# Performance work log

Hardware: AMD Instinct MI355X
Metric: run time of the kernel (lower is better)

The kernel has to match this reference:

```python
import jax, jax.numpy as jnp
from jax import lax
import numpy as np

EPS = 1e-5   # BatchNorm eps (torch default)
LAM = 0.01
W_SIZE = 32768  # window_size; fc_features = W_SIZE - 1


def _conv(x, w, b):
    # torch Conv1d, valid padding; x [N,C,L], w [O,I,K]
    y = lax.conv_general_dilated(x, w, (1,), 'VALID', dimension_numbers=('NCH', 'OIH', 'NCH'))
    return y + b[None, :, None]


def _convT(x, w, b):
    # torch ConvTranspose1d stride 1, pad 0 == full conv with flipped, axis-swapped kernel
    # w [I,O,K] (torch layout) -> [O,I,K] flipped
    k = w.shape[-1]
    wt = jnp.flip(jnp.swapaxes(w, 0, 1), -1)
    y = lax.conv_general_dilated(x, wt, (1,), [(k - 1, k - 1)], dimension_numbers=('NCH', 'OIH', 'NCH'))
    return y + b[None, :, None]


def _bn(x, g, b):
    # BatchNorm1d in training mode: batch stats over (N, L), biased variance
    mu = x.mean((0, 2), keepdims=True)
    var = x.var((0, 2), keepdims=True)
    return g[None, :, None] * (x - mu) * lax.rsqrt(var + EPS) + b[None, :, None]


def setup_inputs() -> dict:
    key = jax.random.key(0)
    ks = jax.random.split(key, 12)
    W = W_SIZE
    F = W - 1
    def w(k, shape):
        return jax.random.normal(k, shape, jnp.float32) * 0.02
    return {
        'x': jax.random.normal(ks[0], (1, 1, 33), jnp.float32),
        'e1_w': w(ks[1], (256, 1, 3)), 'e1_b': jnp.zeros(256),
        'bn2_g': jnp.ones(256), 'bn2_b': jnp.zeros(256),
        'e2_w': w(ks[2], (128, 256, 3)), 'e2_b': jnp.zeros(128),
        'bn3_g': jnp.ones(128), 'bn3_b': jnp.zeros(128),
        'e3_w': w(ks[3], (64, 128, 3)), 'e3_b': jnp.zeros(64),
        'bn4_g': jnp.ones(64), 'bn4_b': jnp.zeros(64),
        'e4_w': w(ks[4], (32, 64, 3)), 'e4_b': jnp.zeros(32),
        'efc_w': w(ks[5], (W, 800)), 'efc_b': jnp.zeros(W),
        'dfc_w': w(ks[6], (800, F)), 'dfc_b': jnp.zeros(800),
        'dbn4_g': jnp.ones(32), 'dbn4_b': jnp.zeros(32),
        'd4_w': w(ks[7], (32, 64, 5)), 'd4_b': jnp.zeros(64),
        'dbn3_g': jnp.ones(64), 'dbn3_b': jnp.zeros(64),
        'd3_w': w(ks[8], (64, 128, 5)), 'd3_b': jnp.zeros(128),
        'dbn2_g': jnp.ones(128), 'dbn2_b': jnp.zeros(128),
        'd2_w': w(ks[9], (128, 256, 5)), 'd2_b': jnp.zeros(256),
        'dbn1_g': jnp.ones(256), 'dbn1_b': jnp.zeros(256),
        'd1_w': w(ks[10], (256, 1, 3)), 'd1_b': jnp.zeros(1),
    }


def reference(x, e1_w, e1_b, bn2_g, bn2_b, e2_w, e2_b, bn3_g, bn3_b, e3_w, e3_b,
              bn4_g, bn4_b, e4_w, e4_b, efc_w, efc_b, dfc_w, dfc_b,
              dbn4_g, dbn4_b, d4_w, d4_b, dbn3_g, dbn3_b, d3_w, d3_b,
              dbn2_g, dbn2_b, d2_w, d2_b, dbn1_g, dbn1_b, d1_w, d1_b):
    # ---- encoder ----
    h = _conv(x, e1_w, e1_b)                                   # [1,256,31]
    h = _conv(jax.nn.relu(_bn(h, bn2_g, bn2_b)), e2_w, e2_b)   # [1,128,29]
    h = _conv(jax.nn.relu(_bn(h, bn3_g, bn3_b)), e3_w, e3_b)   # [1,64,27]
    h = _conv(_bn(jax.nn.relu(h), bn4_g, bn4_b), e4_w, e4_b)   # [1,32,25]
    z = h.reshape(1, -1) @ efc_w.T + efc_b                     # [1, W]
    # ---- calc_Ytilde_prd (no control) ----
    v = z.reshape(-1)
    X, Y = v[:-1], v[1:]                                       # [W-1]
    # m>=n branch: Af = pinv(X^T X + lam) @ X^T Y ; X^T X + lam > 0 so pinv = reciprocal
    Af = jnp.dot(X, Y) / (jnp.dot(X, X) + jnp.asarray(LAM, v.dtype))
    n = X.shape[0]
    # linear scalar recurrence y_i = X[0] * Af^i, vectorized via cumprod
    powers = jnp.cumprod(jnp.concatenate([jnp.ones((1,), v.dtype), jnp.full((n - 1,), Af)]))
    out2 = jnp.stack([X, X[0] * powers], axis=0)               # [2, W-1]
    # ---- decoder ----
    d = out2 @ dfc_w.T + dfc_b                                 # [2, 800]
    d = d.reshape(32, -1)[None]                                # [1,32,50]
    d = _convT(jax.nn.relu(_bn(d, dbn4_g, dbn4_b)), d4_w, d4_b)  # [1,64,54]
    d = _convT(_bn(jax.nn.relu(d), dbn3_g, dbn3_b), d3_w, d3_b)  # [1,128,58]
    d = _convT(_bn(jax.nn.relu(d), dbn2_g, dbn2_b), d2_w, d2_b)  # [1,256,62]
    d = _convT(jax.nn.relu(_bn(d, dbn1_g, dbn1_b)), d1_w, d1_b)  # [1,1,64]
    return jnp.squeeze(d)                                      # [64]
```

## Files before the change

kernel.cpp:

```cpp
#include <hip/hip_runtime.h>
#include <math.h>

#define EPS 1e-5f

__device__ __forceinline__ float waveReduceSum(float v) {
#pragma unroll
    for (int off = 32; off > 0; off >>= 1) v += __shfl_xor(v, off, 64);
    return v;
}

template <int IC, int OC, int LIN, int LOUT, bool BN_FIRST, bool STATS_RELU>
__global__ __launch_bounds__(256) void enc_conv(const float* __restrict__ xin,
                                                const float* __restrict__ g, const float* __restrict__ bb,
                                                const float* __restrict__ s, const float* __restrict__ q,
                                                const float* __restrict__ w, const float* __restrict__ bias,
                                                float* __restrict__ out,
                                                float* __restrict__ so, float* __restrict__ qo) {
    __shared__ float sc[IC], sh[IC];
    int t = threadIdx.x;
    for (int ic = t; ic < IC; ic += 256) {
        float mean = s[ic] / (float)LIN;
        float var = q[ic] / (float)LIN - mean * mean;
        float scale = g[ic] * rsqrtf(var + EPS);
        sc[ic] = scale; sh[ic] = bb[ic] - mean * scale;
    }
    __syncthreads();
    int o = blockIdx.x * 4 + (t >> 6);
    int lane = t & 63;
    if (o >= OC * LOUT) return;
    int oc = o / LOUT, p = o % LOUT;
    constexpr int TERMS = IC * 3;
    const float* wr = w + oc * TERMS;
    float acc = 0.f;
#pragma unroll
    for (int i = 0; i < (TERMS + 63) / 64; i++) {
        int j = 64 * i + lane;
        if ((TERMS & 63) && j >= TERMS) break;
        int ic = j / 3, k = j - ic * 3;
        float xv = xin[ic * LIN + p + k];
        float v;
        if (BN_FIRST) { v = xv * sc[ic] + sh[ic]; v = v > 0.f ? v : 0.f; }
        else          { xv = xv > 0.f ? xv : 0.f; v = xv * sc[ic] + sh[ic]; }
        acc += v * wr[j];
    }
    acc = waveReduceSum(acc);
    if (lane == 0) {
        acc += bias[oc];
        out[oc * LOUT + p] = acc;
        if (so) {
            float r = STATS_RELU ? (acc > 0.f ? acc : 0.f) : acc;
            atomicAdd(&so[oc], r); atomicAdd(&qo[oc], r * r);
        }
    }
}

template <int IC, int OC, int LIN, int LOUT, bool BN_FIRST, bool STATS_RELU>
__global__ __launch_bounds__(256) void dec_convt(const float* __restrict__ xin,
                                                 const float* __restrict__ g, const float* __restrict__ bb,
                                                 const float* __restrict__ s, const float* __restrict__ q,
                                                 const float* __restrict__ w, const float* __restrict__ bias,
                                                 float* __restrict__ out,
                                                 float* __restrict__ so, float* __restrict__ qo) {
    __shared__ float sc[IC], sh[IC];
    int t = threadIdx.x;
    for (int ic = t; ic < IC; ic += 256) {
        float mean = s[ic] / (float)LIN;
        float var = q[ic] / (float)LIN - mean * mean;
        float scale = g[ic] * rsqrtf(var + EPS);
        sc[ic] = scale; sh[ic] = bb[ic] - mean * scale;
    }
    __syncthreads();
    int o = blockIdx.x * 4 + (t >> 6);
    int lane = t & 63;
    if (o >= OC * LOUT) return;
    int oc = o / LOUT, p = o % LOUT;
    constexpr int TERMS = IC * 5;
    float acc = 0.f;
#pragma unroll
    for (int i = 0; i < (TERMS + 63) / 64; i++) {
        int j = 64 * i + lane;
        if ((TERMS & 63) && j >= TERMS) break;
        int ic = j / 5, kk = j - ic * 5;
        int m = p - kk;
        if (m >= 0 && m < LIN) {
            float xv = xin[ic * LIN + m];
            float v;
            if (BN_FIRST) { v = xv * sc[ic] + sh[ic]; v = v > 0.f ? v : 0.f; }
            else          { xv = xv > 0.f ? xv : 0.f; v = xv * sc[ic] + sh[ic]; }
            acc += v * w[ic * (OC * 5) + oc * 5 + kk];
        }
    }
    acc = waveReduceSum(acc);
    if (lane == 0) {
        acc += bias[oc];
        out[oc * LOUT + p] = acc;
        if (so) {
            float r = STATS_RELU ? (acc > 0.f ? acc : 0.f) : acc;
            atomicAdd(&so[oc], r); atomicAdd(&qo[oc], r * r);
        }
    }
}

__global__ __launch_bounds__(256) void k2_enc12(const float* __restrict__ x,
                                                const float* __restrict__ w1,
                                                const float* __restrict__ b1,
                                                const float* __restrict__ g2,
                                                const float* __restrict__ bb2,
                                                const float* __restrict__ w2,
                                                const float* __restrict__ b2,
                                                float* __restrict__ h2,
                                                float* __restrict__ s3, float* __restrict__ q3) {
    __shared__ float xs[33];
    __shared__ float w1l[768];
    __shared__ float b1l[256];
    __shared__ float sc2[256], sh2[256];
    int t = threadIdx.x;
    if (t < 33) xs[t] = x[t];
    for (int i = t; i < 768; i += 256) w1l[i] = w1[i];
    b1l[t] = b1[t];
    __syncthreads();
    {
        float w0 = w1l[t * 3], wa = w1l[t * 3 + 1], wb = w1l[t * 3 + 2], bias = b1l[t];
        float s = 0.f, q = 0.f;
#pragma unroll
        for (int pp = 0; pp < 31; pp++) {
            float v = xs[pp] * w0 + xs[pp + 1] * wa + xs[pp + 2] * wb + bias;
            s += v; q += v * v;
        }
        float mean = s / 31.f;
        float var = q / 31.f - mean * mean;
        float scale = g2[t] * rsqrtf(var + EPS);
        sc2[t] = scale; sh2[t] = bb2[t] - mean * scale;
    }
    __syncthreads();
    int o = blockIdx.x * 4 + (t >> 6);
    int lane = t & 63;
    int oc = o / 29, p = o % 29;
    const float* wr = w2 + oc * 768;
    float acc = 0.f;
#pragma unroll
    for (int i = 0; i < 12; i++) {
        int j = 64 * i + lane;
        int ic = j / 3, k = j - ic * 3;
        int pos = p + k;
        float e1v = xs[pos] * w1l[ic * 3] + xs[pos + 1] * w1l[ic * 3 + 1] + xs[pos + 2] * w1l[ic * 3 + 2] + b1l[ic];
        float v = e1v * sc2[ic] + sh2[ic];
        v = v > 0.f ? v : 0.f;
        acc += v * wr[j];
    }
    acc = waveReduceSum(acc);
    if (lane == 0) {
        acc += b2[oc];
        h2[oc * 29 + p] = acc;
        atomicAdd(&s3[oc], acc);
        atomicAdd(&q3[oc], acc * acc);
    }
}

__global__ __launch_bounds__(256) void k5_gemv1(const float* __restrict__ w,
                                                const float* __restrict__ h,
                                                const float* __restrict__ b,
                                                float* __restrict__ z) {
    int wave = threadIdx.x >> 6;
    int lane = threadIdx.x & 63;
    int row = blockIdx.x * 4 + wave;
    const float4* wr = (const float4*)(w + (size_t)row * 800);
    const float4* hv = (const float4*)h;
    float acc = 0.f;
#pragma unroll
    for (int t = 0; t < 3; t++) {
        float4 a = wr[lane + 64 * t];
        float4 c = hv[lane + 64 * t];
        acc += a.x * c.x + a.y * c.y + a.z * c.z + a.w * c.w;
    }
    if (lane < 8) {
        float4 a = wr[192 + lane];
        float4 c = hv[192 + lane];
        acc += a.x * c.x + a.y * c.y + a.z * c.z + a.w * c.w;
    }
    acc = waveReduceSum(acc);
    if (lane == 0) z[row] = acc + b[row];
}

__global__ __launch_bounds__(1024) void k67_afpow(const float* __restrict__ z, float* __restrict__ pw) {
    int t = threadIdx.x;
    const float4* z4 = (const float4*)z;
    float xy = 0.f, xx = 0.f;
    for (int v = t; v < 8191; v += 1024) {
        float4 a = z4[v];
        float nb = z[4 * v + 4];
        xy += a.x * a.y + a.y * a.z + a.z * a.w + a.w * nb;
        xx += a.x * a.x + a.y * a.y + a.z * a.z + a.w * a.w;
    }
    if (t < 3) {
        int i = 32764 + t;
        xy += z[i] * z[i + 1];
        xx += z[i] * z[i];
    }
    xy = waveReduceSum(xy);
    xx = waveReduceSum(xx);
    __shared__ float sx[16], sy[16];
    __shared__ float afs;
    int wv = t >> 6, ln = t & 63;
    if (ln == 0) { sy[wv] = xy; sx[wv] = xx; }
    __syncthreads();
    if (t == 0) {
        float SY = 0.f, SX = 0.f;
        for (int i = 0; i < 16; i++) { SY += sy[i]; SX += sx[i]; }
        afs = SY / (SX + 0.01f);
    }
    __syncthreads();
    float base0 = afs;
    float4* pw4 = (float4*)pw;
    for (int v = t; v < 8192; v += 1024) {
        float4 r;
        float* rp = (float*)&r;
#pragma unroll
        for (int u = 0; u < 4; u++) {
            int e = 4 * v + u;
            float rr = 1.f, base = base0;
            while (e) { if (e & 1) rr *= base; base *= base; e >>= 1; }
            rp[u] = rr;
        }
        pw4[v] = r;
    }
}

__global__ __launch_bounds__(256) void k8_gemv2(const float* __restrict__ w,
                                                const float* __restrict__ z,
                                                const float* __restrict__ pw,
                                                const float* __restrict__ b,
                                                float* __restrict__ d,
                                                float* __restrict__ s, float* __restrict__ q) {
    int j = blockIdx.x;
    int t = threadIdx.x;
    const float* wr = w + (size_t)j * 32767;
    int head = j & 3;
    float a0 = 0.f, a1 = 0.f;
    if (t < head) { float wv = wr[t]; a0 += z[t] * wv; a1 += pw[t] * wv; }
    int n4 = (32767 - head) >> 2;
    const float4* wv4 = (const float4*)(wr + head);
    for (int v = t; v < n4; v += 256) {
        float4 a = wv4[v];
        int i = head + 4 * v;
        a0 += z[i] * a.x + z[i + 1] * a.y + z[i + 2] * a.z + z[i + 3] * a.w;
        a1 += pw[i] * a.x + pw[i + 1] * a.y + pw[i + 2] * a.z + pw[i + 3] * a.w;
    }
    int tail = (32767 - head) & 3;
    int tstart = head + 4 * n4;
    if (t < tail) { int i = tstart + t; float wv = wr[i]; a0 += z[i] * wv; a1 += pw[i] * wv; }

    a0 = waveReduceSum(a0);
    a1 = waveReduceSum(a1);
    __shared__ float r0[4], r1[4];
    int wave = t >> 6, lane = t & 63;
    if (lane == 0) { r0[wave] = a0; r1[wave] = a1; }
    __syncthreads();
    if (t == 0) {
        float d0 = r0[0] + r0[1] + r0[2] + r0[3] + b[j];
        float d1 = z[0] * (r1[0] + r1[1] + r1[2] + r1[3]) + b[j];
        d[j] = d0;
        d[800 + j] = d1;
        int c0 = j / 50, c1 = 16 + j / 50;
        atomicAdd(&s[c0], d0); atomicAdd(&q[c0], d0 * d0);
        atomicAdd(&s[c1], d1); atomicAdd(&q[c1], d1 * d1);
    }
}

__global__ __launch_bounds__(256) void k12_dec1(const float* __restrict__ h6,
                                                const float* __restrict__ g, const float* __restrict__ bb,
                                                const float* __restrict__ s, const float* __restrict__ q,
                                                const float* __restrict__ w, const float* __restrict__ b1,
                                                float* __restrict__ out) {
    __shared__ float sc[256], sh[256];
    int t = threadIdx.x;
    {
        float mean = s[t] / 62.f;
        float var = q[t] / 62.f - mean * mean;
        float scale = g[t] * rsqrtf(var + EPS);
        sc[t] = scale; sh[t] = bb[t] - mean * scale;
    }
    __syncthreads();
    int p = blockIdx.x * 4 + (t >> 6);
    int lane = t & 63;
    float acc = 0.f;
#pragma unroll
    for (int i = 0; i < 12; i++) {
        int j = 64 * i + lane;
        int ic = j / 3, kk = j - ic * 3;
        int m = p - kk;
        if (m >= 0 && m < 62) {
            float v = h6[ic * 62 + m] * sc[ic] + sh[ic];
            v = v > 0.f ? v : 0.f;
            acc += v * w[j];
        }
    }
    acc = waveReduceSum(acc);
    if (lane == 0) out[p] = acc + b1[0];
}

extern "C" void kernel_launch(void* const* d_in, const int* in_sizes, int n_in,
                              void* d_out, int out_size, void* d_ws, size_t ws_size,
                              hipStream_t stream) {
    const float* x      = (const float*)d_in[0];
    const float* e1_w   = (const float*)d_in[1];
    const float* e1_b   = (const float*)d_in[2];
    const float* bn2_g  = (const float*)d_in[3];
    const float* bn2_b  = (const float*)d_in[4];
    const float* e2_w   = (const float*)d_in[5];
    const float* e2_b   = (const float*)d_in[6];
    const float* bn3_g  = (const float*)d_in[7];
    const float* bn3_b  = (const float*)d_in[8];
    const float* e3_w   = (const float*)d_in[9];
    const float* e3_b   = (const float*)d_in[10];
    const float* bn4_g  = (const float*)d_in[11];
    const float* bn4_b  = (const float*)d_in[12];
    const float* e4_w   = (const float*)d_in[13];
    const float* e4_b   = (const float*)d_in[14];
    const float* efc_w  = (const float*)d_in[15];
    const float* efc_b  = (const float*)d_in[16];
    const float* dfc_w  = (const float*)d_in[17];
    const float* dfc_b  = (const float*)d_in[18];
    const float* dbn4_g = (const float*)d_in[19];
    const float* dbn4_b = (const float*)d_in[20];
    const float* d4_w   = (const float*)d_in[21];
    const float* d4_b   = (const float*)d_in[22];
    const float* dbn3_g = (const float*)d_in[23];
    const float* dbn3_b = (const float*)d_in[24];
    const float* d3_w   = (const float*)d_in[25];
    const float* d3_b   = (const float*)d_in[26];
    const float* dbn2_g = (const float*)d_in[27];
    const float* dbn2_b = (const float*)d_in[28];
    const float* d2_w   = (const float*)d_in[29];
    const float* d2_b   = (const float*)d_in[30];
    const float* dbn1_g = (const float*)d_in[31];
    const float* dbn1_b = (const float*)d_in[32];
    const float* d1_w   = (const float*)d_in[33];
    const float* d1_b   = (const float*)d_in[34];
    float* out = (float*)d_out;

    float* W = (float*)d_ws;
    float* bn3s  = W + 0;    float* bn3q  = W + 128;
    float* bn4s  = W + 256;  float* bn4q  = W + 320;
    float* dbn4s = W + 384;  float* dbn4q = W + 416;
    float* dbn3s = W + 448;  float* dbn3q = W + 512;
    float* dbn2s = W + 576;  float* dbn2q = W + 704;
    float* dbn1s = W + 832;  float* dbn1q = W + 1088;
    float* h2    = W + 1344;
    float* h3    = W + 5056;
    float* h800  = W + 6784;
    float* z     = W + 7584;
    float* pw    = W + 40352;
    float* dvec  = W + 73120;
    float* h4    = W + 74720;
    float* h5    = W + 78176;
    float* h6    = W + 85600;

    hipMemsetAsync(d_ws, 0, 1344 * sizeof(float), stream);

    k2_enc12<<<928, 256, 0, stream>>>(x, e1_w, e1_b, bn2_g, bn2_b, e2_w, e2_b, h2, bn3s, bn3q);
    enc_conv<128, 64, 29, 27, true, true><<<432, 256, 0, stream>>>(
        h2, bn3_g, bn3_b, bn3s, bn3q, e3_w, e3_b, h3, bn4s, bn4q);
    enc_conv<64, 32, 27, 25, false, false><<<200, 256, 0, stream>>>(
        h3, bn4_g, bn4_b, bn4s, bn4q, e4_w, e4_b, h800, nullptr, nullptr);
    k5_gemv1<<<8192, 256, 0, stream>>>(efc_w, h800, efc_b, z);
    k67_afpow<<<1, 1024, 0, stream>>>(z, pw);
    k8_gemv2<<<800, 256, 0, stream>>>(dfc_w, z, pw, dfc_b, dvec, dbn4s, dbn4q);
    dec_convt<32, 64, 50, 54, true, true><<<864, 256, 0, stream>>>(
        dvec, dbn4_g, dbn4_b, dbn4s, dbn4q, d4_w, d4_b, h4, dbn3s, dbn3q);
    dec_convt<64, 128, 54, 58, false, true><<<1856, 256, 0, stream>>>(
        h4, dbn3_g, dbn3_b, dbn3s, dbn3q, d3_w, d3_b, h5, dbn2s, dbn2q);
    dec_convt<128, 256, 58, 62, false, false><<<3968, 256, 0, stream>>>(
        h5, dbn2_g, dbn2_b, dbn2s, dbn2q, d2_w, d2_b, h6, dbn1s, dbn1q);
    k12_dec1<<<16, 256, 0, stream>>>(h6, dbn1_g, dbn1_b, dbn1s, dbn1q, d1_w, d1_b, out);
}
```

Baseline: 506.1 us.

## Restructure conv kernels: stage normalized input in LDS, one wave per output channel

```diff
diff --git a/kernel.cpp b/kernel.cpp
--- a/kernel.cpp
+++ b/kernel.cpp
@@ -9,14 +9,16 @@
     return v;
 }
 
-template <int IC, int OC, int LIN, int LOUT, bool BN_FIRST, bool STATS_RELU>
-__global__ __launch_bounds__(256) void enc_conv(const float* __restrict__ xin,
-                                                const float* __restrict__ g, const float* __restrict__ bb,
-                                                const float* __restrict__ s, const float* __restrict__ q,
-                                                const float* __restrict__ w, const float* __restrict__ bias,
-                                                float* __restrict__ out,
-                                                float* __restrict__ so, float* __restrict__ qo) {
+template <int IC, int OC, int LIN, bool BN_FIRST, bool HAS_STATS, bool STATS_RELU>
+__global__ __launch_bounds__(256) void enc_conv2(const float* __restrict__ xin,
+                                                 const float* __restrict__ g, const float* __restrict__ bb,
+                                                 const float* __restrict__ s, const float* __restrict__ q,
+                                                 const float* __restrict__ w, const float* __restrict__ bias,
+                                                 float* __restrict__ out,
+                                                 float* __restrict__ so, float* __restrict__ qo) {
+    constexpr int LOUT = LIN - 2;
     __shared__ float sc[IC], sh[IC];
+    __shared__ float xn[IC * LIN];
     int t = threadIdx.x;
     for (int ic = t; ic < IC; ic += 256) {
         float mean = s[ic] / (float)LIN;
@@ -25,43 +27,46 @@
         sc[ic] = scale; sh[ic] = bb[ic] - mean * scale;
     }
     __syncthreads();
-    int o = blockIdx.x * 4 + (t >> 6);
-    int lane = t & 63;
-    if (o >= OC * LOUT) return;
-    int oc = o / LOUT, p = o % LOUT;
-    constexpr int TERMS = IC * 3;
-    const float* wr = w + oc * TERMS;
-    float acc = 0.f;
-#pragma unroll
-    for (int i = 0; i < (TERMS + 63) / 64; i++) {
-        int j = 64 * i + lane;
-        if ((TERMS & 63) && j >= TERMS) break;
-        int ic = j / 3, k = j - ic * 3;
-        float xv = xin[ic * LIN + p + k];
+    for (int i = t; i < IC * LIN; i += 256) {
+        int ic = i / LIN;
+        float xv = xin[i];
         float v;
-        if (BN_FIRST) { v = xv * sc[ic] + sh[ic]; v = v > 0.f ? v : 0.f; }
-        else          { xv = xv > 0.f ? xv : 0.f; v = xv * sc[ic] + sh[ic]; }
-        acc += v * wr[j];
-    }
-    acc = waveReduceSum(acc);
-    if (lane == 0) {
-        acc += bias[oc];
-        out[oc * LOUT + p] = acc;
-        if (so) {
-            float r = STATS_RELU ? (acc > 0.f ? acc : 0.f) : acc;
-            atomicAdd(&so[oc], r); atomicAdd(&qo[oc], r * r);
-        }
-    }
-}
-
-template <int IC, int OC, int LIN, int LOUT, bool BN_FIRST, bool STATS_RELU>
-__global__ __launch_bounds__(256) void dec_convt(const float* __restrict__ xin,
-                                                 const float* __restrict__ g, const float* __restrict__ bb,
-                                                 const float* __restrict__ s, const float* __restrict__ q,
-                                                 const float* __restrict__ w, const float* __restrict__ bias,
-                                                 float* __restrict__ out,
-                                                 float* __restrict__ so, float* __restrict__ qo) {
+        if (BN_FIRST) { v = xv * sc[ic] + sh[ic]; v = fmaxf(v, 0.f); }
+        else          { xv = fmaxf(xv, 0.f); v = xv * sc[ic] + sh[ic]; }
+        xn[i] = v;
+    }
+    __syncthreads();
+    int oc = blockIdx.x * 4 + (t >> 6);
+    int p0 = t & 63;
+    int p = p0 < LOUT ? p0 : 0;
+    const float* woc = w + oc * (IC * 3);
+    float acc = 0.f;
+#pragma unroll 8
+    for (int ic = 0; ic < IC; ic++) {
+        const float* xi = xn + ic * LIN;
+        const float* wi = woc + ic * 3;
+        acc += xi[p] * wi[0] + xi[p + 1] * wi[1] + xi[p + 2] * wi[2];
+    }
+    float val = acc + bias[oc];
+    if constexpr (HAS_STATS) {
+        float r = (p0 < LOUT) ? (STATS_RELU ? fmaxf(val, 0.f) : val) : 0.f;
+        float ssum = waveReduceSum(r);
+        float qsum = waveReduceSum(r * r);
+        if (p0 == 0) { so[oc] = ssum; qo[oc] = qsum; }
+    }
+    if (p0 < LOUT) out[oc * LOUT + p0] = val;
+}
+
+template <int IC, int OC, int LIN, bool BN_FIRST, bool HAS_STATS, bool STATS_RELU>
+__global__ __launch_bounds__(256) void dec_convt2(const float* __restrict__ xin,
+                                                  const float* __restrict__ g, const float* __restrict__ bb,
+                                                  const float* __restrict__ s, const float* __restrict__ q,
+                                                  const float* __restrict__ w, const float* __restrict__ bias,
+                                                  float* __restrict__ out,
+                                                  float* __restrict__ so, float* __restrict__ qo) {
+    constexpr int LOUT = LIN + 4;
     __shared__ float sc[IC], sh[IC];
+    __shared__ float xn[IC * LIN];
     int t = threadIdx.x;
     for (int ic = t; ic < IC; ic += 256) {
         float mean = s[ic] / (float)LIN;
@@ -70,35 +75,38 @@
         sc[ic] = scale; sh[ic] = bb[ic] - mean * scale;
     }
     __syncthreads();
-    int o = blockIdx.x * 4 + (t >> 6);
-    int lane = t & 63;
-    if (o >= OC * LOUT) return;
-    int oc = o / LOUT, p = o % LOUT;
-    constexpr int TERMS = IC * 5;
-    float acc = 0.f;
-#pragma unroll
-    for (int i = 0; i < (TERMS + 63) / 64; i++) {
-        int j = 64 * i + lane;
-        if ((TERMS & 63) && j >= TERMS) break;
-        int ic = j / 5, kk = j - ic * 5;
-        int m = p - kk;
-        if (m >= 0 && m < LIN) {
-            float xv = xin[ic * LIN + m];
-            float v;
-            if (BN_FIRST) { v = xv * sc[ic] + sh[ic]; v = v > 0.f ? v : 0.f; }
-            else          { xv = xv > 0.f ? xv : 0.f; v = xv * sc[ic] + sh[ic]; }
-            acc += v * w[ic * (OC * 5) + oc * 5 + kk];
-        }
-    }
-    acc = waveReduceSum(acc);
-    if (lane == 0) {
-        acc += bias[oc];
-        out[oc * LOUT + p] = acc;
-        if (so) {
-            float r = STATS_RELU ? (acc > 0.f ? acc : 0.f) : acc;
-            atomicAdd(&so[oc], r); atomicAdd(&qo[oc], r * r);
-        }
-    }
+    for (int i = t; i < IC * LIN; i += 256) {
+        int ic = i / LIN;
+        float xv = xin[i];
+        float v;
+        if (BN_FIRST) { v = xv * sc[ic] + sh[ic]; v = fmaxf(v, 0.f); }
+        else          { xv = fmaxf(xv, 0.f); v = xv * sc[ic] + sh[ic]; }
+        xn[i] = v;
+    }
+    __syncthreads();
+    int oc = blockIdx.x * 4 + (t >> 6);
+    int p = t & 63;
+    const float* woc = w + oc * 5;
+    float acc = 0.f;
+#pragma unroll 8
+    for (int ic = 0; ic < IC; ic++) {
+        const float* wi = woc + ic * (OC * 5);
+        const float* xi = xn + ic * LIN;
+#pragma unroll
+        for (int kk = 0; kk < 5; kk++) {
+            int m = p - kk;
+            float xv = (m >= 0 && m < LIN) ? xi[m] : 0.f;
+            acc += xv * wi[kk];
+        }
+    }
+    float val = acc + bias[oc];
+    if constexpr (HAS_STATS) {
+        float r = (p < LOUT) ? (STATS_RELU ? fmaxf(val, 0.f) : val) : 0.f;
+        float ssum = waveReduceSum(r);
+        float qsum = waveReduceSum(r * r);
+        if (p == 0) { so[oc] = ssum; qo[oc] = qsum; }
+    }
+    if (p < LOUT) out[oc * LOUT + p] = val;
 }
 
 __global__ __launch_bounds__(256) void k2_enc12(const float* __restrict__ x,
@@ -111,50 +119,47 @@
                                                 float* __restrict__ h2,
                                                 float* __restrict__ s3, float* __restrict__ q3) {
     __shared__ float xs[33];
-    __shared__ float w1l[768];
-    __shared__ float b1l[256];
-    __shared__ float sc2[256], sh2[256];
+    __shared__ float e1n[256 * 33];
     int t = threadIdx.x;
     if (t < 33) xs[t] = x[t];
-    for (int i = t; i < 768; i += 256) w1l[i] = w1[i];
-    b1l[t] = b1[t];
     __syncthreads();
     {
-        float w0 = w1l[t * 3], wa = w1l[t * 3 + 1], wb = w1l[t * 3 + 2], bias = b1l[t];
+        float w0 = w1[t * 3], wa = w1[t * 3 + 1], wb = w1[t * 3 + 2], bias = b1[t];
+        float vals[31];
         float s = 0.f, q = 0.f;
 #pragma unroll
         for (int pp = 0; pp < 31; pp++) {
             float v = xs[pp] * w0 + xs[pp + 1] * wa + xs[pp + 2] * wb + bias;
-            s += v; q += v * v;
+            vals[pp] = v; s += v; q += v * v;
         }
         float mean = s / 31.f;
         float var = q / 31.f - mean * mean;
         float scale = g2[t] * rsqrtf(var + EPS);
-        sc2[t] = scale; sh2[t] = bb2[t] - mean * scale;
-    }
-    __syncthreads();
-    int o = blockIdx.x * 4 + (t >> 6);
-    int lane = t & 63;
-    int oc = o / 29, p = o % 29;
-    const float* wr = w2 + oc * 768;
-    float acc = 0.f;
-#pragma unroll
-    for (int i = 0; i < 12; i++) {
-        int j = 64 * i + lane;
-        int ic = j / 3, k = j - ic * 3;
-        int pos = p + k;
-        float e1v = xs[pos] * w1l[ic * 3] + xs[pos + 1] * w1l[ic * 3 + 1] + xs[pos + 2] * w1l[ic * 3 + 2] + b1l[ic];
-        float v = e1v * sc2[ic] + sh2[ic];
-        v = v > 0.f ? v : 0.f;
-        acc += v * wr[j];
-    }
-    acc = waveReduceSum(acc);
-    if (lane == 0) {
-        acc += b2[oc];
-        h2[oc * 29 + p] = acc;
-        atomicAdd(&s3[oc], acc);
-        atomicAdd(&q3[oc], acc * acc);
-    }
+        float shift = bb2[t] - mean * scale;
+#pragma unroll
+        for (int pp = 0; pp < 31; pp++) {
+            float v = vals[pp] * scale + shift;
+            e1n[t * 33 + pp] = fmaxf(v, 0.f);
+        }
+    }
+    __syncthreads();
+    int oc = blockIdx.x * 4 + (t >> 6);
+    int p0 = t & 63;
+    int p = p0 < 29 ? p0 : 0;
+    const float* woc = w2 + oc * 768;
+    float acc = 0.f;
+#pragma unroll 8
+    for (int ic = 0; ic < 256; ic++) {
+        const float* xi = e1n + ic * 33;
+        const float* wi = woc + ic * 3;
+        acc += xi[p] * wi[0] + xi[p + 1] * wi[1] + xi[p + 2] * wi[2];
+    }
+    float val = acc + b2[oc];
+    float r = (p0 < 29) ? val : 0.f;
+    float ssum = waveReduceSum(r);
+    float qsum = waveReduceSum(r * r);
+    if (p0 == 0) { s3[oc] = ssum; q3[oc] = qsum; }
+    if (p0 < 29) h2[oc * 29 + p0] = val;
 }
 
 __global__ __launch_bounds__(256) void k5_gemv1(const float* __restrict__ w,
@@ -291,7 +296,7 @@
         int m = p - kk;
         if (m >= 0 && m < 62) {
             float v = h6[ic * 62 + m] * sc[ic] + sh[ic];
-            v = v > 0.f ? v : 0.f;
+            v = fmaxf(v, 0.f);
             acc += v * w[j];
         }
     }
@@ -358,19 +363,19 @@
 
     hipMemsetAsync(d_ws, 0, 1344 * sizeof(float), stream);
 
-    k2_enc12<<<928, 256, 0, stream>>>(x, e1_w, e1_b, bn2_g, bn2_b, e2_w, e2_b, h2, bn3s, bn3q);
-    enc_conv<128, 64, 29, 27, true, true><<<432, 256, 0, stream>>>(
+    k2_enc12<<<32, 256, 0, stream>>>(x, e1_w, e1_b, bn2_g, bn2_b, e2_w, e2_b, h2, bn3s, bn3q);
+    enc_conv2<128, 64, 29, true, true, true><<<16, 256, 0, stream>>>(
         h2, bn3_g, bn3_b, bn3s, bn3q, e3_w, e3_b, h3, bn4s, bn4q);
-    enc_conv<64, 32, 27, 25, false, false><<<200, 256, 0, stream>>>(
+    enc_conv2<64, 32, 27, false, false, false><<<8, 256, 0, stream>>>(
         h3, bn4_g, bn4_b, bn4s, bn4q, e4_w, e4_b, h800, nullptr, nullptr);
     k5_gemv1<<<8192, 256, 0, stream>>>(efc_w, h800, efc_b, z);
     k67_afpow<<<1, 1024, 0, stream>>>(z, pw);
     k8_gemv2<<<800, 256, 0, stream>>>(dfc_w, z, pw, dfc_b, dvec, dbn4s, dbn4q);
-    dec_convt<32, 64, 50, 54, true, true><<<864, 256, 0, stream>>>(
+    dec_convt2<32, 64, 50, true, true, true><<<16, 256, 0, stream>>>(
         dvec, dbn4_g, dbn4_b, dbn4s, dbn4q, d4_w, d4_b, h4, dbn3s, dbn3q);
-    dec_convt<64, 128, 54, 58, false, true><<<1856, 256, 0, stream>>>(
+    dec_convt2<64, 128, 54, false, true, true><<<32, 256, 0, stream>>>(
         h4, dbn3_g, dbn3_b, dbn3s, dbn3q, d3_w, d3_b, h5, dbn2s, dbn2q);
-    dec_convt<128, 256, 58, 62, false, false><<<3968, 256, 0, stream>>>(
+    dec_convt2<128, 256, 58, false, true, false><<<64, 256, 0, stream>>>(
         h5, dbn2_g, dbn2_b, dbn2s, dbn2q, d2_w, d2_b, h6, dbn1s, dbn1q);
     k12_dec1<<<16, 256, 0, stream>>>(h6, dbn1_g, dbn1_b, dbn1s, dbn1q, d1_w, d1_b, out);
 }
```

After: 420.1 us. 1.2x faster.
